# Optimization experiments

Measured on AMD Instinct MI355X. Metric: run time of the kernel, lower is better.

The kernel has to match this reference:

```python
import jax, jax.numpy as jnp
import numpy as np

DIM = 768
NUM_BLOCKS = 4
BLOCK = DIM // NUM_BLOCKS
SCALE = 0.02
LAMBDA = 0.01
EPS = 1e-5


def setup_inputs() -> dict:
    key = jax.random.key(0)
    ks = jax.random.split(key, 6)
    B, H, W = 64, 32, 32
    x = jax.random.normal(ks[0], (B, DIM, H, W), dtype=jnp.float32)
    w1 = jax.random.normal(ks[1], (2, NUM_BLOCKS, BLOCK, BLOCK), dtype=jnp.float32) * SCALE
    w2 = jax.random.normal(ks[2], (2, NUM_BLOCKS, BLOCK, BLOCK), dtype=jnp.float32) * SCALE
    b1 = jax.random.normal(ks[3], (2, NUM_BLOCKS, BLOCK), dtype=jnp.float32) * SCALE
    b2 = jax.random.normal(ks[4], (2, NUM_BLOCKS, BLOCK), dtype=jnp.float32) * SCALE
    gamma = jnp.ones((DIM,), dtype=jnp.float32)
    beta = jnp.zeros((DIM,), dtype=jnp.float32)
    return {"x": x, "w1": w1, "w2": w2, "b1": b1, "b2": b2,
            "gamma": gamma, "beta": beta, "H": H, "W": W}


def _softshrink(s, lam):
    return jnp.where(s > lam, s - lam, jnp.where(s < -lam, s + lam, jnp.zeros_like(s)))


def reference(x, w1, w2, b1, b2, gamma, beta, H, W):
    B, C = x.shape[0], x.shape[1]
    nb, bs = NUM_BLOCKS, C // NUM_BLOCKS
    # (B, C, H, W) -> (B, N, C)
    xt = x.reshape(B, C, H * W).transpose(0, 2, 1)
    residual = xt
    # LayerNorm over channel dim
    mu = jnp.mean(xt, axis=-1, keepdims=True)
    var = jnp.mean(jnp.square(xt - mu), axis=-1, keepdims=True)
    xn = (xt - mu) / jnp.sqrt(var + EPS) * gamma + beta
    # (B, N, nb, bs), FFT2 over (N, nb)
    xf = jnp.fft.fft2(xn.reshape(B, H * W, nb, bs), axes=(1, 2), norm='ortho')
    xr, xi = xf.real, xf.imag

    def mul(u, w):
        return jnp.einsum('bnqd,qdk->bnqk', u, w)  # block-diagonal matmul

    r1 = jax.nn.relu(mul(xr, w1[0]) - mul(xi, w1[1]) + b1[0])
    i1 = jax.nn.relu(mul(xr, w1[1]) + mul(xi, w1[0]) + b1[1])
    r2 = mul(r1, w2[0]) - mul(i1, w2[1]) + b2[0]
    i2 = mul(r1, w2[1]) + mul(i1, w2[0]) + b2[1]
    s = jnp.stack([r2, i2], axis=-1)
    s = _softshrink(s, LAMBDA)
    xc = jax.lax.complex(s[..., 0], s[..., 1])
    y = jnp.fft.ifft2(xc, axes=(1, 2), norm='ortho').real  # cast complex->real keeps real part
    y = y.reshape(B, H * W, C) + residual
    return y.transpose(0, 2, 1).reshape(B, C, H, W)
```

## Files before the change

### kernel.cpp

```cpp
#include <hip/hip_runtime.h>
#include <math.h>

#define BB 64
#define CC 768
#define NN 1024
#define BS 192
#define EPS 1e-5f
#define LAM 0.01f

typedef float  f32x4  __attribute__((ext_vector_type(4)));
typedef short  bf16x8 __attribute__((ext_vector_type(8)));

__device__ inline unsigned f2bf(float x) {
    unsigned u = __float_as_uint(x);
    u += 0x7fff + ((u >> 16) & 1);
    return u >> 16;
}
__device__ inline unsigned pack2(float r, float i) { return f2bf(r) | (f2bf(i) << 16); }
__device__ inline float bflo(unsigned v) { return __uint_as_float(v << 16); }
__device__ inline float bfhi(unsigned v) { return __uint_as_float(v & 0xffff0000u); }

__device__ inline int swz(int i) { return i ^ (((i >> 4) & 3) << 2); }

__device__ inline int rev4(int p) {
    return ((p & 3) << 8) | ((p & 12) << 4) | (p & 48) | ((p >> 4) & 12) | ((p >> 8) & 3);
}
__device__ inline int prt(int p) {
    return rev4((1024 - rev4(p)) & 1023);
}
__device__ inline float2 cmul(float2 z, float c, float s) {
    return make_float2(z.x * c - z.y * s, z.x * s + z.y * c);
}

__global__ __launch_bounds__(512) void ln_stats(const float* __restrict__ x,
                                                float* __restrict__ mu,
                                                float* __restrict__ rstd) {
    int tn = threadIdx.x & 63, tc = threadIdx.x >> 6;
    int n = blockIdx.x * 256 + tn * 4, b = blockIdx.y;
    const float* xp = x + (size_t)b * CC * NN + n;
    f32x4 s = (f32x4)0.f, ss = (f32x4)0.f;
    #pragma unroll 4
    for (int c = tc; c < CC; c += 8) {
        f32x4 v = *(const f32x4*)(xp + (size_t)c * NN);
        s += v; ss += v * v;
    }
    __shared__ f32x4 sm[8][64], sq[8][64];
    sm[tc][tn] = s; sq[tc][tn] = ss;
    __syncthreads();
    if (tc == 0) {
        f32x4 S  = sm[0][tn], SS = sq[0][tn];
        #pragma unroll
        for (int i = 1; i < 8; i++) { S += sm[i][tn]; SS += sq[i][tn]; }
        f32x4 m = S * (1.f / 768.f);
        f32x4 r;
        #pragma unroll
        for (int i = 0; i < 4; i++) {
            float var = SS[i] * (1.f / 768.f) - m[i] * m[i];
            r[i] = rsqrtf(var + EPS);
        }
        *(f32x4*)(mu + (size_t)b * NN + n)   = m;
        *(f32x4*)(rstd + (size_t)b * NN + n) = r;
    }
}

__global__ void fwd_fft(const float* __restrict__ x,
                        const float* __restrict__ mu_, const float* __restrict__ rs_,
                        const float* __restrict__ gamma, const float* __restrict__ beta,
                        unsigned* __restrict__ Xp) {
    __shared__ float2 bufs[2][1024];
    int d = blockIdx.x, b = blockIdx.y, tid = threadIdx.x;
    int n0 = 4 * tid;
    int i0 = swz(n0);

    f32x4 mu4 = *(const f32x4*)(mu_ + (size_t)b * NN + n0);
    f32x4 rs4 = *(const f32x4*)(rs_ + (size_t)b * NN + n0);
    f32x4 xq[4];
    #pragma unroll
    for (int q = 0; q < 4; q++) {
        int c = q * BS + d;
        float g = gamma[c], be = beta[c];
        f32x4 v = *(const f32x4*)(x + ((size_t)b * CC + c) * NN + n0);
        #pragma unroll
        for (int j = 0; j < 4; j++)
            v[j] = (v[j] - mu4[j]) * rs4[j] * g + be;
        xq[q] = v;
    }
    #pragma unroll
    for (int j = 0; j < 4; j++) {
        float a = xq[0][j], b1v = xq[1][j], c2v = xq[2][j], d3v = xq[3][j];
        bufs[0][i0 + j] = make_float2(a + b1v + c2v + d3v, a - b1v + c2v - d3v);
        bufs[1][i0 + j] = make_float2(a - c2v, d3v - b1v);
    }
    __syncthreads();

    #pragma unroll
    for (int sL = 0; sL < 4; sL++) {
        const int L = 256 >> (2 * sL);
        int j = tid & (L - 1);
        int base = ((tid - j) << 2) + j;
        float s1, c1;
        __sincosf(-(float)M_PI * 0.5f * (float)j / (float)L, &s1, &c1);
        float c2 = c1 * c1 - s1 * s1, s2 = 2.f * c1 * s1;
        float c3 = c2 * c1 - s2 * s1, s3 = c2 * s1 + s2 * c1;
        #pragma unroll
        for (int pl = 0; pl < 2; pl++) {
            float2 a  = bufs[pl][swz(base)];
            float2 bb = bufs[pl][swz(base + L)];
            float2 cc = bufs[pl][swz(base + 2 * L)];
            float2 dd = bufs[pl][swz(base + 3 * L)];
            float t0r = a.x + cc.x, t0i = a.y + cc.y;
            float t1r = a.x - cc.x, t1i = a.y - cc.y;
            float t2r = bb.x + dd.x, t2i = bb.y + dd.y;
            float t3r = bb.x - dd.x, t3i = bb.y - dd.y;
            float X0r = t0r + t2r, X0i = t0i + t2i;
            float X2r = t0r - t2r, X2i = t0i - t2i;
            float X1r = t1r + t3i, X1i = t1i - t3r;
            float X3r = t1r - t3i, X3i = t1i + t3r;
            bufs[pl][swz(base)]         = make_float2(X0r, X0i);
            bufs[pl][swz(base + L)]     = make_float2(X1r * c1 - X1i * s1, X1r * s1 + X1i * c1);
            bufs[pl][swz(base + 2 * L)] = make_float2(X2r * c2 - X2i * s2, X2r * s2 + X2i * c2);
            bufs[pl][swz(base + 3 * L)] = make_float2(X3r * c3 - X3i * s3, X3r * s3 + X3i * c3);
        }
        __syncthreads();
    }

    float2 A[2][4];
    #pragma unroll
    for (int pl = 0; pl < 2; pl++) {
        const float4* p4 = (const float4*)&bufs[pl][i0];
        float4 v0 = p4[0], v1 = p4[1];
        float t0r = v0.x + v1.x, t0i = v0.y + v1.y;
        float t1r = v0.x - v1.x, t1i = v0.y - v1.y;
        float t2r = v0.z + v1.z, t2i = v0.w + v1.w;
        float t3r = v0.z - v1.z, t3i = v0.w - v1.w;
        A[pl][0] = make_float2(t0r + t2r, t0i + t2i);
        A[pl][1] = make_float2(t1r + t3i, t1i - t3r);
        A[pl][2] = make_float2(t0r - t2r, t0i - t2i);
        A[pl][3] = make_float2(t1r - t3i, t1i + t3r);
    }
    #pragma unroll
    for (int pl = 0; pl < 2; pl++)
        #pragma unroll
        for (int j = 0; j < 4; j++)
            bufs[pl][i0 + j] = A[pl][j];
    __syncthreads();

    const float sc  = 1.f / 64.f;
    const float sc2 = 1.f / 128.f;
    unsigned o0[4], o1[4], o2[4], o3[4];
    #pragma unroll
    for (int j = 0; j < 4; j++) {
        int p = n0 + j;
        int pq = prt(p);
        float2 zap = A[0][j], zbp = A[1][j];
        float2 zaq = bufs[0][swz(pq)];
        float2 zbq = bufs[1][swz(pq)];
        float p0r = zap.x + zaq.x, p0i = zap.y - zaq.y;
        float dr  = zap.x - zaq.x, di  = zap.y + zaq.y;
        o0[j] = pack2(p0r * sc2, p0i * sc2);
        o2[j] = pack2(di * sc2, -dr * sc2);
        o1[j] = pack2(zbp.x * sc, zbp.y * sc);
        o3[j] = pack2(zbq.x * sc, -zbq.y * sc);
    }
    size_t qs = (size_t)BS * NN;
    size_t base = (((size_t)b * 4) * BS + d) * NN + n0;
    *(uint4*)(Xp + base)          = make_uint4(o0[0], o0[1], o0[2], o0[3]);
    *(uint4*)(Xp + base + qs)     = make_uint4(o1[0], o1[1], o1[2], o1[3]);
    *(uint4*)(Xp + base + 2 * qs) = make_uint4(o2[0], o2[1], o2[2], o2[3]);
    *(uint4*)(Xp + base + 3 * qs) = make_uint4(o3[0], o3[1], o3[2], o3[3]);
}

__global__ void pack_b(const float* __restrict__ w, unsigned* __restrict__ Bp) {
    int ch = blockIdx.x, q = blockIdx.y;
    const float* wr = w + (size_t)q * BS * BS;
    const float* wi = w + (size_t)(4 + q) * BS * BS;
    size_t base = ((size_t)q * 12 + ch) * (384 * 16);
    for (int r = 0; r < 24; r++) {
        int idx = r * 256 + threadIdx.x;
        int j = idx >> 4, dd = idx & 15;
        int h = j >> 1;
        int dg = ch * 16 + dd;
        float Wr = wr[(size_t)dg * BS + h];
        float Wi = wi[(size_t)dg * BS + h];
        Bp[base + idx] = (j & 1) ? pack2(Wi, Wr) : pack2(Wr, -Wi);
    }
}

__global__ __launch_bounds__(512) void fused_mlp(const unsigned* __restrict__ Ap,
                                                 const unsigned* __restrict__ Bp1,
                                                 const unsigned* __restrict__ Bp2,
                                                 const float* __restrict__ b1,
                                                 const float* __restrict__ b2,
                                                 unsigned* __restrict__ Yp) {
    __shared__ __align__(16) unsigned tl[12288];

    const int mblk = blockIdx.x;
    const int bq   = blockIdx.y;
    const int q    = bq & 3;
    const int tid  = threadIdx.x;
    const int wave = tid >> 6;
    const int lane = tid & 63;
    const int l15  = lane & 15;
    const int quad = lane >> 4;
    const int jw   = wave * 48;

    const size_t bstride = 384 * 16;
    const unsigned* b1_lane = Bp1 + (size_t)q * 12 * bstride + (jw + l15) * 16 + quad * 4;
    const unsigned* b2_lane = Bp2 + (size_t)q * 12 * bstride + (jw + l15) * 16 + quad * 4;

    {
        const unsigned* abase = Ap + ((size_t)bq * BS) * NN + (size_t)mblk * 64;
        unsigned st[24];
        #pragma unroll
        for (int i = 0; i < 6; i++) {
            int r = (i * 8 + wave) * 4 + quad;
            const unsigned* gp = abase + (size_t)r * NN + l15;
            #pragma unroll
            for (int k = 0; k < 4; k++) st[i * 4 + k] = gp[16 * k];
        }
        #pragma unroll
        for (int i = 0; i < 6; i++) {
            int s = i * 8 + wave;
            unsigned* lp = &tl[s * 256 + quad];
            #pragma unroll
            for (int k = 0; k < 4; k++) lp[(l15 + 16 * k) * 4] = st[i * 4 + k];
        }
    }

    f32x4 acc[3][4];
    #pragma unroll
    for (int i = 0; i < 3; i++)
        #pragma unroll
        for (int j = 0; j < 4; j++)
            acc[i][j] = (f32x4)0.f;

    __syncthreads();

    for (int ch = 0; ch < 12; ch++) {
        const unsigned* tp = &tl[(ch * 4 + quad) * 256];
        const unsigned* bp = b1_lane + ch * bstride;
        bf16x8 af[4], bfr[3];
        #pragma unroll
        for (int tm = 0; tm < 4; tm++)
            af[tm] = *(const bf16x8*)(tp + (tm * 16 + l15) * 4);
        #pragma unroll
        for (int tn = 0; tn < 3; tn++) {
            union { uint4 u4; bf16x8 v; } bu;
            bu.u4 = *(const uint4*)(bp + tn * 256);
            bfr[tn] = bu.v;
        }
        #pragma unroll
        for (int tn = 0; tn < 3; tn++)
            #pragma unroll
            for (int tm = 0; tm < 4; tm++)
                acc[tn][tm] = __builtin_amdgcn_mfma_f32_16x16x32_bf16(bfr[tn], af[tm], acc[tn][tm], 0, 0, 0);
    }

    __syncthreads();

    #pragma unroll
    for (int tn = 0; tn < 3; tn++) {
        int hg = (jw >> 1) + tn * 8 + quad * 2;
        float b0r = b1[q * BS + hg];
        float b0i = b1[768 + q * BS + hg];
        float b1r_ = b1[q * BS + hg + 1];
        float b1i_ = b1[768 + q * BS + hg + 1];
        #pragma unroll
        for (int tm = 0; tm < 4; tm++) {
            int c = tm * 16 + l15;
            f32x4 a = acc[tn][tm];
            float v0 = fmaxf(a[0] + b0r, 0.f);
            float v1 = fmaxf(a[1] + b0i, 0.f);
            float v2 = fmaxf(a[2] + b1r_, 0.f);
            float v3 = fmaxf(a[3] + b1i_, 0.f);
            unsigned* hp = &tl[(hg >> 2) * 256 + c * 4 + (hg & 3)];
            *(uint2*)hp = make_uint2(pack2(v0, v1), pack2(v2, v3));
            acc[tn][tm] = (f32x4)0.f;
        }
    }
    __syncthreads();

    for (int ch = 0; ch < 12; ch++) {
        const unsigned* tp = &tl[(ch * 4 + quad) * 256];
        const unsigned* bp = b2_lane + ch * bstride;
        bf16x8 af[4], bfr[3];
        #pragma unroll
        for (int tm = 0; tm < 4; tm++)
            af[tm] = *(const bf16x8*)(tp + (tm * 16 + l15) * 4);
        #pragma unroll
        for (int tn = 0; tn < 3; tn++) {
            union { uint4 u4; bf16x8 v; } bu;
            bu.u4 = *(const uint4*)(bp + tn * 256);
            bfr[tn] = bu.v;
        }
        #pragma unroll
        for (int tn = 0; tn < 3; tn++)
            #pragma unroll
            for (int tm = 0; tm < 4; tm++)
                acc[tn][tm] = __builtin_amdgcn_mfma_f32_16x16x32_bf16(bfr[tn], af[tm], acc[tn][tm], 0, 0, 0);
    }

    #pragma unroll
    for (int tn = 0; tn < 3; tn++) {
        int hg = (jw >> 1) + tn * 8 + quad * 2;
        float b0r = b2[q * BS + hg];
        float b0i = b2[768 + q * BS + hg];
        float b1r_ = b2[q * BS + hg + 1];
        float b1i_ = b2[768 + q * BS + hg + 1];
        size_t row0 = ((size_t)bq * BS + hg) * NN + (size_t)mblk * 64;
        #pragma unroll
        for (int tm = 0; tm < 4; tm++) {
            int mcol = tm * 16 + l15;
            f32x4 a = acc[tn][tm];
            float v0 = a[0] + b0r, v1 = a[1] + b0i;
            float v2 = a[2] + b1r_, v3 = a[3] + b1i_;
            v0 = (v0 > LAM) ? (v0 - LAM) : ((v0 < -LAM) ? (v0 + LAM) : 0.f);
            v1 = (v1 > LAM) ? (v1 - LAM) : ((v1 < -LAM) ? (v1 + LAM) : 0.f);
            v2 = (v2 > LAM) ? (v2 - LAM) : ((v2 < -LAM) ? (v2 + LAM) : 0.f);
            v3 = (v3 > LAM) ? (v3 - LAM) : ((v3 < -LAM) ? (v3 + LAM) : 0.f);
            Yp[row0 + mcol]      = pack2(v0, v1);
            Yp[row0 + NN + mcol] = pack2(v2, v3);
        }
    }
}

__global__ void inv_fft(const float* __restrict__ x,
                        const unsigned* __restrict__ Yp,
                        float* __restrict__ out) {
    __shared__ float2 bufs[4][1024];
    int d = blockIdx.x, b = blockIdx.y, tid = threadIdx.x;
    int n0 = 4 * tid;
    int i0 = swz(n0);

    float2 S[4][4];
    size_t qs = (size_t)BS * NN;
    size_t rowb = (((size_t)b * 4) * BS + d) * NN + n0;
    #pragma unroll
    for (int u = 0; u < 4; u++) {
        uint4 v = *(const uint4*)(Yp + rowb + (size_t)u * qs);
        S[u][0] = make_float2(bflo(v.x), bfhi(v.x));
        S[u][1] = make_float2(bflo(v.y), bfhi(v.y));
        S[u][2] = make_float2(bflo(v.z), bfhi(v.z));
        S[u][3] = make_float2(bflo(v.w), bfhi(v.w));
    }
    #pragma unroll
    for (int u = 0; u < 4; u++)
        #pragma unroll
        for (int j = 0; j < 4; j++)
            bufs[u][i0 + j] = S[u][j];
    __syncthreads();

    float2 Wa[4], Wb[4];
    #pragma unroll
    for (int j = 0; j < 4; j++) {
        int p = n0 + j;
        int pq = prt(p);
        float2 s0q = bufs[0][swz(pq)];
        float2 s2q = bufs[2][swz(pq)];
        float2 s3q = bufs[3][swz(pq)];
        float h0r = S[0][j].x + s0q.x, h0i = S[0][j].y - s0q.y;
        float h2r = S[2][j].x + s2q.x, h2i = S[2][j].y - s2q.y;
        Wa[j] = make_float2(h0r - h2i, h0i + h2r);
        Wb[j] = make_float2(S[1][j].x + s3q.x, S[1][j].y - s3q.y);
    }
    __syncthreads();

    #pragma unroll
    for (int pl = 0; pl < 2; pl++) {
        float2 w0 = pl ? Wb[0] : Wa[0], w1 = pl ? Wb[1] : Wa[1];
        float2 w2 = pl ? Wb[2] : Wa[2], w3 = pl ? Wb[3] : Wa[3];
        float t0r = w0.x + w2.x, t0i = w0.y + w2.y;
        float t1r = w0.x - w2.x, t1i = w0.y - w2.y;
        float t2r = w1.x + w3.x, t2i = w1.y + w3.y;
        float t3r = w1.x - w3.x, t3i = w1.y - w3.y;
        bufs[pl][i0 + 0] = make_float2(t0r + t2r, t0i + t2i);
        bufs[pl][i0 + 1] = make_float2(t1r - t3i, t1i + t3r);
        bufs[pl][i0 + 2] = make_float2(t0r - t2r, t0i - t2i);
        bufs[pl][i0 + 3] = make_float2(t1r + t3i, t1i - t3r);
    }
    __syncthreads();

    #pragma unroll
    for (int sL = 0; sL < 4; sL++) {
        const int L = 4 << (2 * sL);
        int j = tid & (L - 1);
        int base = ((tid - j) << 2) + j;
        float s1, c1;
        __sincosf((float)M_PI * 0.5f * (float)j / (float)L, &s1, &c1);
        float c2 = c1 * c1 - s1 * s1, s2 = 2.f * c1 * s1;
        float c3 = c2 * c1 - s2 * s1, s3 = c2 * s1 + s2 * c1;
        #pragma unroll
        for (int pl = 0; pl < 2; pl++) {
            float2 y0 = bufs[pl][swz(base)];
            float2 y1 = bufs[pl][swz(base + L)];
            float2 y2 = bufs[pl][swz(base + 2 * L)];
            float2 y3 = bufs[pl][swz(base + 3 * L)];
            float A1r = y1.x * c1 - y1.y * s1, A1i = y1.x * s1 + y1.y * c1;
            float A2r = y2.x * c2 - y2.y * s2, A2i = y2.x * s2 + y2.y * c2;
            float A3r = y3.x * c3 - y3.y * s3, A3i = y3.x * s3 + y3.y * c3;
            float t0r = y0.x + A2r, t0i = y0.y + A2i;
            float t1r = y0.x - A2r, t1i = y0.y - A2i;
            float t2r = A1r + A3r, t2i = A1i + A3i;
            float t3r = A1r - A3r, t3i = A1i - A3i;
            bufs[pl][swz(base)]         = make_float2(t0r + t2r, t0i + t2i);
            bufs[pl][swz(base + L)]     = make_float2(t1r - t3i, t1i + t3r);
            bufs[pl][swz(base + 2 * L)] = make_float2(t0r - t2r, t0i - t2i);
            bufs[pl][swz(base + 3 * L)] = make_float2(t1r + t3i, t1i - t3r);
        }
        __syncthreads();
    }

    float2 Va[4], Vb[4];
    {
        const float4* pa = (const float4*)&bufs[0][i0];
        const float4* pb = (const float4*)&bufs[1][i0];
        float4 a0 = pa[0], a1 = pa[1], b0 = pb[0], b1v = pb[1];
        Va[0] = make_float2(a0.x, a0.y); Va[1] = make_float2(a0.z, a0.w);
        Va[2] = make_float2(a1.x, a1.y); Va[3] = make_float2(a1.z, a1.w);
        Vb[0] = make_float2(b0.x, b0.y); Vb[1] = make_float2(b0.z, b0.w);
        Vb[2] = make_float2(b1v.x, b1v.y); Vb[3] = make_float2(b1v.z, b1v.w);
    }
    const float sc = 1.f / 128.f;
    f32x4 y0v, y1v, y2v, y3v;
    #pragma unroll
    for (int j = 0; j < 4; j++) {
        float V0 = Va[j].x, V2 = Va[j].y;
        float R1 = Vb[j].x, I1 = Vb[j].y;
        y0v[j] = (V0 + V2 + 2.f * R1) * sc;
        y1v[j] = (V0 - V2 - 2.f * I1) * sc;
        y2v[j] = (V0 + V2 - 2.f * R1) * sc;
        y3v[j] = (V0 - V2 + 2.f * I1) * sc;
    }
    size_t row0 = (((size_t)b * 4 + 0) * BS + d) * NN + n0;
    size_t row1 = (((size_t)b * 4 + 1) * BS + d) * NN + n0;
    size_t row2 = (((size_t)b * 4 + 2) * BS + d) * NN + n0;
    size_t row3 = (((size_t)b * 4 + 3) * BS + d) * NN + n0;
    f32x4 x0 = *(const f32x4*)(x + row0);
    f32x4 x1 = *(const f32x4*)(x + row1);
    f32x4 x2 = *(const f32x4*)(x + row2);
    f32x4 x3 = *(const f32x4*)(x + row3);
    *(f32x4*)(out + row0) = y0v + x0;
    *(f32x4*)(out + row1) = y1v + x1;
    *(f32x4*)(out + row2) = y2v + x2;
    *(f32x4*)(out + row3) = y3v + x3;
}

extern "C" void kernel_launch(void* const* d_in, const int* in_sizes, int n_in,
                              void* d_out, int out_size, void* d_ws, size_t ws_size,
                              hipStream_t stream) {
    const float* x     = (const float*)d_in[0];
    const float* w1    = (const float*)d_in[1];
    const float* w2    = (const float*)d_in[2];
    const float* b1    = (const float*)d_in[3];
    const float* b2    = (const float*)d_in[4];
    const float* gamma = (const float*)d_in[5];
    const float* beta  = (const float*)d_in[6];

    unsigned* Xp = (unsigned*)d_ws;
    float* mu    = (float*)d_ws + (size_t)BB * CC * NN;
    float* rstd  = mu + (size_t)BB * NN;
    unsigned* Bp1 = (unsigned*)(rstd + (size_t)BB * NN);
    unsigned* Bp2 = Bp1 + (size_t)4 * 12 * 384 * 16;
    unsigned* Yp = Xp;

    pack_b<<<dim3(12, 4), 256, 0, stream>>>(w1, Bp1);
    pack_b<<<dim3(12, 4), 256, 0, stream>>>(w2, Bp2);
    ln_stats<<<dim3(NN / 256, BB), 512, 0, stream>>>(x, mu, rstd);
    fwd_fft<<<dim3(BS, BB), 256, 0, stream>>>(x, mu, rstd, gamma, beta, Xp);
    fused_mlp<<<dim3(16, 256), 512, 0, stream>>>(Xp, Bp1, Bp2, b1, b2, Yp);
    inv_fft<<<dim3(BS, BB), 256, 0, stream>>>(x, Yp, (float*)d_out);
}
```

Before: 688.0 us.

## Process two channels per fwd_fft block, add MFMA priority, shrink inv_fft LDS

Each fwd_fft workgroup now transforms two channel columns, halving the grid and sharing the mu/rstd loads and twiddle computation across four FFT planes. The fused MLP brackets its MFMA loops with s_setprio to favor matrix issue over other waves. inv_fft drops one unused LDS plane (S[1] was never read back from shared memory), cutting its LDS footprint to raise occupancy. The wider fwd_fft uses double the LDS and more registers, which may lower its occupancy.

Result: no change. 699.5 us (+1.7%).

```diff
diff --git a/kernel.cpp b/kernel.cpp
--- a/kernel.cpp
+++ b/kernel.cpp
@@ -67,29 +67,33 @@
                         const float* __restrict__ mu_, const float* __restrict__ rs_,
                         const float* __restrict__ gamma, const float* __restrict__ beta,
                         unsigned* __restrict__ Xp) {
-    __shared__ float2 bufs[2][1024];
-    int d = blockIdx.x, b = blockIdx.y, tid = threadIdx.x;
+    __shared__ float2 bufs[4][1024];
+    int d0 = blockIdx.x * 2, b = blockIdx.y, tid = threadIdx.x;
     int n0 = 4 * tid;
     int i0 = swz(n0);
 
     f32x4 mu4 = *(const f32x4*)(mu_ + (size_t)b * NN + n0);
     f32x4 rs4 = *(const f32x4*)(rs_ + (size_t)b * NN + n0);
-    f32x4 xq[4];
-    #pragma unroll
-    for (int q = 0; q < 4; q++) {
-        int c = q * BS + d;
-        float g = gamma[c], be = beta[c];
-        f32x4 v = *(const f32x4*)(x + ((size_t)b * CC + c) * NN + n0);
-        #pragma unroll
-        for (int j = 0; j < 4; j++)
-            v[j] = (v[j] - mu4[j]) * rs4[j] * g + be;
-        xq[q] = v;
-    }
-    #pragma unroll
-    for (int j = 0; j < 4; j++) {
-        float a = xq[0][j], b1v = xq[1][j], c2v = xq[2][j], d3v = xq[3][j];
-        bufs[0][i0 + j] = make_float2(a + b1v + c2v + d3v, a - b1v + c2v - d3v);
-        bufs[1][i0 + j] = make_float2(a - c2v, d3v - b1v);
+    #pragma unroll
+    for (int dd = 0; dd < 2; dd++) {
+        int d = d0 + dd;
+        f32x4 xq[4];
+        #pragma unroll
+        for (int q = 0; q < 4; q++) {
+            int c = q * BS + d;
+            float g = gamma[c], be = beta[c];
+            f32x4 v = *(const f32x4*)(x + ((size_t)b * CC + c) * NN + n0);
+            #pragma unroll
+            for (int j = 0; j < 4; j++)
+                v[j] = (v[j] - mu4[j]) * rs4[j] * g + be;
+            xq[q] = v;
+        }
+        #pragma unroll
+        for (int j = 0; j < 4; j++) {
+            float a = xq[0][j], b1v = xq[1][j], c2v = xq[2][j], d3v = xq[3][j];
+            bufs[2 * dd][i0 + j]     = make_float2(a + b1v + c2v + d3v, a - b1v + c2v - d3v);
+            bufs[2 * dd + 1][i0 + j] = make_float2(a - c2v, d3v - b1v);
+        }
     }
     __syncthreads();
 
@@ -103,7 +107,7 @@
         float c2 = c1 * c1 - s1 * s1, s2 = 2.f * c1 * s1;
         float c3 = c2 * c1 - s2 * s1, s3 = c2 * s1 + s2 * c1;
         #pragma unroll
-        for (int pl = 0; pl < 2; pl++) {
+        for (int pl = 0; pl < 4; pl++) {
             float2 a  = bufs[pl][swz(base)];
             float2 bb = bufs[pl][swz(base + L)];
             float2 cc = bufs[pl][swz(base + 2 * L)];
@@ -124,50 +128,57 @@
         __syncthreads();
     }
 
-    float2 A[2][4];
-    #pragma unroll
-    for (int pl = 0; pl < 2; pl++) {
-        const float4* p4 = (const float4*)&bufs[pl][i0];
-        float4 v0 = p4[0], v1 = p4[1];
-        float t0r = v0.x + v1.x, t0i = v0.y + v1.y;
-        float t1r = v0.x - v1.x, t1i = v0.y - v1.y;
-        float t2r = v0.z + v1.z, t2i = v0.w + v1.w;
-        float t3r = v0.z - v1.z, t3i = v0.w - v1.w;
-        A[pl][0] = make_float2(t0r + t2r, t0i + t2i);
-        A[pl][1] = make_float2(t1r + t3i, t1i - t3r);
-        A[pl][2] = make_float2(t0r - t2r, t0i - t2i);
-        A[pl][3] = make_float2(t1r - t3i, t1i + t3r);
-    }
-    #pragma unroll
-    for (int pl = 0; pl < 2; pl++)
-        #pragma unroll
-        for (int j = 0; j < 4; j++)
-            bufs[pl][i0 + j] = A[pl][j];
+    float2 A[2][2][4];
+    #pragma unroll
+    for (int dd = 0; dd < 2; dd++)
+        #pragma unroll
+        for (int pl = 0; pl < 2; pl++) {
+            const float4* p4 = (const float4*)&bufs[2 * dd + pl][i0];
+            float4 v0 = p4[0], v1 = p4[1];
+            float t0r = v0.x + v1.x, t0i = v0.y + v1.y;
+            float t1r = v0.x - v1.x, t1i = v0.y - v1.y;
+            float t2r = v0.z + v1.z, t2i = v0.w + v1.w;
+            float t3r = v0.z - v1.z, t3i = v0.w - v1.w;
+            A[dd][pl][0] = make_float2(t0r + t2r, t0i + t2i);
+            A[dd][pl][1] = make_float2(t1r + t3i, t1i - t3r);
+            A[dd][pl][2] = make_float2(t0r - t2r, t0i - t2i);
+            A[dd][pl][3] = make_float2(t1r - t3i, t1i + t3r);
+        }
+    #pragma unroll
+    for (int dd = 0; dd < 2; dd++)
+        #pragma unroll
+        for (int pl = 0; pl < 2; pl++)
+            #pragma unroll
+            for (int j = 0; j < 4; j++)
+                bufs[2 * dd + pl][i0 + j] = A[dd][pl][j];
     __syncthreads();
 
     const float sc  = 1.f / 64.f;
     const float sc2 = 1.f / 128.f;
-    unsigned o0[4], o1[4], o2[4], o3[4];
-    #pragma unroll
-    for (int j = 0; j < 4; j++) {
-        int p = n0 + j;
-        int pq = prt(p);
-        float2 zap = A[0][j], zbp = A[1][j];
-        float2 zaq = bufs[0][swz(pq)];
-        float2 zbq = bufs[1][swz(pq)];
-        float p0r = zap.x + zaq.x, p0i = zap.y - zaq.y;
-        float dr  = zap.x - zaq.x, di  = zap.y + zaq.y;
-        o0[j] = pack2(p0r * sc2, p0i * sc2);
-        o2[j] = pack2(di * sc2, -dr * sc2);
-        o1[j] = pack2(zbp.x * sc, zbp.y * sc);
-        o3[j] = pack2(zbq.x * sc, -zbq.y * sc);
-    }
     size_t qs = (size_t)BS * NN;
-    size_t base = (((size_t)b * 4) * BS + d) * NN + n0;
-    *(uint4*)(Xp + base)          = make_uint4(o0[0], o0[1], o0[2], o0[3]);
-    *(uint4*)(Xp + base + qs)     = make_uint4(o1[0], o1[1], o1[2], o1[3]);
-    *(uint4*)(Xp + base + 2 * qs) = make_uint4(o2[0], o2[1], o2[2], o2[3]);
-    *(uint4*)(Xp + base + 3 * qs) = make_uint4(o3[0], o3[1], o3[2], o3[3]);
+    #pragma unroll
+    for (int dd = 0; dd < 2; dd++) {
+        unsigned o0[4], o1[4], o2[4], o3[4];
+        #pragma unroll
+        for (int j = 0; j < 4; j++) {
+            int p = n0 + j;
+            int pq = prt(p);
+            float2 zap = A[dd][0][j], zbp = A[dd][1][j];
+            float2 zaq = bufs[2 * dd][swz(pq)];
+            float2 zbq = bufs[2 * dd + 1][swz(pq)];
+            float p0r = zap.x + zaq.x, p0i = zap.y - zaq.y;
+            float dr  = zap.x - zaq.x, di  = zap.y + zaq.y;
+            o0[j] = pack2(p0r * sc2, p0i * sc2);
+            o2[j] = pack2(di * sc2, -dr * sc2);
+            o1[j] = pack2(zbp.x * sc, zbp.y * sc);
+            o3[j] = pack2(zbq.x * sc, -zbq.y * sc);
+        }
+        size_t base = (((size_t)b * 4) * BS + (d0 + dd)) * NN + n0;
+        *(uint4*)(Xp + base)          = make_uint4(o0[0], o0[1], o0[2], o0[3]);
+        *(uint4*)(Xp + base + qs)     = make_uint4(o1[0], o1[1], o1[2], o1[3]);
+        *(uint4*)(Xp + base + 2 * qs) = make_uint4(o2[0], o2[1], o2[2], o2[3]);
+        *(uint4*)(Xp + base + 3 * qs) = make_uint4(o3[0], o3[1], o3[2], o3[3]);
+    }
 }
 
 __global__ void pack_b(const float* __restrict__ w, unsigned* __restrict__ Bp) {
@@ -249,11 +260,13 @@
             bu.u4 = *(const uint4*)(bp + tn * 256);
             bfr[tn] = bu.v;
         }
+        __builtin_amdgcn_s_setprio(1);
         #pragma unroll
         for (int tn = 0; tn < 3; tn++)
             #pragma unroll
             for (int tm = 0; tm < 4; tm++)
                 acc[tn][tm] = __builtin_amdgcn_mfma_f32_16x16x32_bf16(bfr[tn], af[tm], acc[tn][tm], 0, 0, 0);
+        __builtin_amdgcn_s_setprio(0);
     }
 
     __syncthreads();
@@ -293,11 +306,13 @@
             bu.u4 = *(const uint4*)(bp + tn * 256);
             bfr[tn] = bu.v;
         }
+        __builtin_amdgcn_s_setprio(1);
         #pragma unroll
         for (int tn = 0; tn < 3; tn++)
             #pragma unroll
             for (int tm = 0; tm < 4; tm++)
                 acc[tn][tm] = __builtin_amdgcn_mfma_f32_16x16x32_bf16(bfr[tn], af[tm], acc[tn][tm], 0, 0, 0);
+        __builtin_amdgcn_s_setprio(0);
     }
 
     #pragma unroll
@@ -327,7 +342,7 @@
 __global__ void inv_fft(const float* __restrict__ x,
                         const unsigned* __restrict__ Yp,
                         float* __restrict__ out) {
-    __shared__ float2 bufs[4][1024];
+    __shared__ float2 bufs[3][1024];
     int d = blockIdx.x, b = blockIdx.y, tid = threadIdx.x;
     int n0 = 4 * tid;
     int i0 = swz(n0);
@@ -344,10 +359,11 @@
         S[u][3] = make_float2(bflo(v.w), bfhi(v.w));
     }
     #pragma unroll
-    for (int u = 0; u < 4; u++)
-        #pragma unroll
-        for (int j = 0; j < 4; j++)
-            bufs[u][i0 + j] = S[u][j];
+    for (int j = 0; j < 4; j++) {
+        bufs[0][i0 + j] = S[0][j];
+        bufs[1][i0 + j] = S[2][j];
+        bufs[2][i0 + j] = S[3][j];
+    }
     __syncthreads();
 
     float2 Wa[4], Wb[4];
@@ -356,8 +372,8 @@
         int p = n0 + j;
         int pq = prt(p);
         float2 s0q = bufs[0][swz(pq)];
-        float2 s2q = bufs[2][swz(pq)];
-        float2 s3q = bufs[3][swz(pq)];
+        float2 s2q = bufs[1][swz(pq)];
+        float2 s3q = bufs[2][swz(pq)];
         float h0r = S[0][j].x + s0q.x, h0i = S[0][j].y - s0q.y;
         float h2r = S[2][j].x + s2q.x, h2i = S[2][j].y - s2q.y;
         Wa[j] = make_float2(h0r - h2i, h0i + h2r);
@@ -466,7 +482,7 @@
     pack_b<<<dim3(12, 4), 256, 0, stream>>>(w1, Bp1);
     pack_b<<<dim3(12, 4), 256, 0, stream>>>(w2, Bp2);
     ln_stats<<<dim3(NN / 256, BB), 512, 0, stream>>>(x, mu, rstd);
-    fwd_fft<<<dim3(BS, BB), 256, 0, stream>>>(x, mu, rstd, gamma, beta, Xp);
+    fwd_fft<<<dim3(BS / 2, BB), 256, 0, stream>>>(x, mu, rstd, gamma, beta, Xp);
     fused_mlp<<<dim3(16, 256), 512, 0, stream>>>(Xp, Bp1, Bp2, b1, b2, Yp);
     inv_fft<<<dim3(BS, BB), 256, 0, stream>>>(x, Yp, (float*)d_out);
 }
```
